# Optimization experiments

Hardware: AMD Instinct MI355X
Metric: run time of the kernel (lower is better)

Reference implementation:

```python
import jax, jax.numpy as jnp
import numpy as np


def setup_inputs() -> dict:
    key = jax.random.key(0)
    k1, k2, k3 = jax.random.split(key, 3)
    B, N, L, H, E = 4, 4, 1024, 8, 64
    queries = jax.random.normal(k1, (B, N, L, H, E), dtype=jnp.float32)
    keys = jax.random.normal(k2, (B, N, L, H, E), dtype=jnp.float32)
    values = jax.random.normal(k3, (B, N, L, H, E), dtype=jnp.float32)
    return {"queries": queries, "keys": keys, "values": values}


def reference(queries, keys, values):
    B, N, L, H, E = queries.shape
    S = values.shape[2]
    scale = 1.0 / jnp.sqrt(jnp.asarray(E, queries.dtype))
    # scores: [B, N, H, L, S]
    scores = jnp.einsum('bnlhe,bnshe->bnhls', queries, keys)
    # causal mask: True above the diagonal (future positions), broadcast over b,n,h
    causal = jnp.triu(jnp.ones((L, S), dtype=bool), k=1)
    scores = jnp.where(causal, -jnp.inf, scores)
    A = jax.nn.softmax(scale * scores, axis=-1)  # dropout p=0.0 -> identity
    V = jnp.einsum('bnhls,bnshd->bnlhd', A, values)
    return V
```

## Files before the change

### kernel.cpp

```cpp
#include <hip/hip_runtime.h>
#include <hip/hip_bf16.h>


typedef __bf16 bf16x8 __attribute__((ext_vector_type(8)));
typedef __bf16 bf16x4 __attribute__((ext_vector_type(4)));
typedef float  f32x4  __attribute__((ext_vector_type(4)));
typedef unsigned u32x2 __attribute__((ext_vector_type(2)));
typedef unsigned u32x4 __attribute__((ext_vector_type(4)));

#define SEQ 1024
#define ROWSTRIDE 512

__device__ inline bf16x8 pack8(float4 a, float4 b) {
    bf16x8 f;
    f[0]=(__bf16)a.x; f[1]=(__bf16)a.y; f[2]=(__bf16)a.z; f[3]=(__bf16)a.w;
    f[4]=(__bf16)b.x; f[5]=(__bf16)b.y; f[6]=(__bf16)b.z; f[7]=(__bf16)b.w;
    return f;
}

__device__ inline bf16x8 pack8s(float4 a, float4 b, float s) {
    bf16x8 f;
    f[0]=(__bf16)(a.x*s); f[1]=(__bf16)(a.y*s); f[2]=(__bf16)(a.z*s); f[3]=(__bf16)(a.w*s);
    f[4]=(__bf16)(b.x*s); f[5]=(__bf16)(b.y*s); f[6]=(__bf16)(b.z*s); f[7]=(__bf16)(b.w*s);
    return f;
}

__device__ inline void lds_barrier() {
    asm volatile("s_waitcnt lgkmcnt(0)\n\ts_barrier" ::: "memory");
}

__device__ inline void swap32(unsigned &a, unsigned &b) {
    asm("v_permlane32_swap_b32 %0, %1" : "+v"(a), "+v"(b));
}
__device__ inline void swap16(unsigned &a, unsigned &b) {
    asm("v_permlane16_swap_b32 %0, %1" : "+v"(a), "+v"(b));
}

__global__ __launch_bounds__(256) void attn_fwd(
    const float* __restrict__ Qg,
    const float* __restrict__ Kg,
    const float* __restrict__ Vg,
    float* __restrict__ Og)
{
    __shared__ __bf16 Kds[2][64][64];
    __shared__ __bf16 Vds[2][64][64];

    const int blk  = blockIdx.x;
    const int qt   = blk >> 7;
    const int head = blk & 127;
    const int h    = head & 7;
    const int bn   = head >> 3;

    const int tid  = threadIdx.x;
    const int wave = tid >> 6;
    const int lane = tid & 63;
    const int quad = lane >> 4;
    const int l15  = lane & 15;
    const int swz  = l15 & 7;

    const size_t base = (size_t)bn * SEQ * ROWSTRIDE + (size_t)h * 64;

    const float kscale = 0.125f * 1.44269504088896f;

    const int qrow = qt * 128 + wave * 32;
    bf16x8 qa[2][2];
    #pragma unroll
    for (int qh = 0; qh < 2; ++qh) {
        const float* qp = Qg + base + (size_t)(qrow + qh * 16 + l15) * ROWSTRIDE + quad * 8;
        #pragma unroll
        for (int t = 0; t < 2; ++t)
            qa[qh][t] = pack8s(*(const float4*)(qp + t * 32),
                               *(const float4*)(qp + t * 32 + 4), kscale);
    }

    f32x4 o[2][4];
    float lsum[2] = {0.f, 0.f};
    #pragma unroll
    for (int qh = 0; qh < 2; ++qh)
        #pragma unroll
        for (int e = 0; e < 4; ++e) o[qh][e] = (f32x4){0.f, 0.f, 0.f, 0.f};

    const int sr = tid >> 2, cbk = (tid & 3) << 1;
    const int ve = tid & 63, cbv = (tid >> 6) << 1;

    const int ntiles = 2 * qt + 2;

    const float* kp = Kg + base + (size_t)sr * ROWSTRIDE + (cbk << 3);
    const float* vp = Vg + base + (size_t)(cbv << 3) * ROWSTRIDE + ve;

    float4 kpre[4];
    float  vpre[16];
    #pragma unroll
    for (int i = 0; i < 4; ++i) kpre[i] = *(const float4*)(kp + i * 4);
    #pragma unroll
    for (int j = 0; j < 16; ++j) vpre[j] = vp[(size_t)j * ROWSTRIDE];
    kp += (size_t)64 * ROWSTRIDE;
    vp += (size_t)64 * ROWSTRIDE;

    for (int tile = 0; tile < ntiles; ++tile) {
        const int bb = tile & 1;

        {
            const int rk = sr & 7;
            *(bf16x8*)&Kds[bb][sr][(cbk ^ rk) << 3]       = pack8(kpre[0], kpre[1]);
            *(bf16x8*)&Kds[bb][sr][((cbk + 1) ^ rk) << 3] = pack8(kpre[2], kpre[3]);
            bf16x8 f0, f1;
            #pragma unroll
            for (int jj = 0; jj < 8; ++jj) { f0[jj] = (__bf16)vpre[jj]; f1[jj] = (__bf16)vpre[8 + jj]; }
            const int rv = ve & 7;
            *(bf16x8*)&Vds[bb][ve][(cbv ^ rv) << 3]       = f0;
            *(bf16x8*)&Vds[bb][ve][((cbv + 1) ^ rv) << 3] = f1;
        }

        if (tile + 1 < ntiles) {
            #pragma unroll
            for (int i = 0; i < 4; ++i) kpre[i] = *(const float4*)(kp + i * 4);
            #pragma unroll
            for (int j = 0; j < 16; ++j) vpre[j] = vp[(size_t)j * ROWSTRIDE];
            kp += (size_t)64 * ROWSTRIDE;
            vp += (size_t)64 * ROWSTRIDE;
        }

        lds_barrier();

        const int relq = tile * 64 - qrow;
        const bool active   = relq < 32;
        const bool hiActive = relq < 0;

        bf16x8 pf[2][2];

        auto phase = [&](int ph) {
            f32x4 sacc[2][2];
            #pragma unroll
            for (int qh = 0; qh < 2; ++qh)
                #pragma unroll
                for (int cl = 0; cl < 2; ++cl) sacc[qh][cl] = (f32x4){0.f, 0.f, 0.f, 0.f};
            __builtin_amdgcn_s_setprio(1);
            #pragma unroll
            for (int cl = 0; cl < 2; ++cl) {
                #pragma unroll
                for (int t = 0; t < 2; ++t) {
                    bf16x8 kb = *(const bf16x8*)&Kds[bb][(ph * 2 + cl) * 16 + l15][((t * 4 + quad) ^ swz) << 3];
                    sacc[0][cl] = __builtin_amdgcn_mfma_f32_16x16x32_bf16(kb, qa[0][t], sacc[0][cl], 0, 0, 0);
                    sacc[1][cl] = __builtin_amdgcn_mfma_f32_16x16x32_bf16(kb, qa[1][t], sacc[1][cl], 0, 0, 0);
                }
            }
            __builtin_amdgcn_s_setprio(0);
            const int pm = relq + ph * 32;
            #pragma unroll
            for (int qh = 0; qh < 2; ++qh) {
                unsigned U[2][2];
                float ls = 0.f;
                if (pm == 0) {
                    #pragma unroll
                    for (int cl = 0; cl < 2; ++cl) {
                        bf16x4 pk;
                        #pragma unroll
                        for (int r = 0; r < 4; ++r) {
                            float p = __builtin_amdgcn_exp2f(sacc[qh][cl][r]);
                            if (cl * 16 + quad * 4 + r > qh * 16 + l15) p = 0.f;
                            ls += p; pk[r] = (__bf16)p;
                        }
                        u32x2 uu = __builtin_bit_cast(u32x2, pk);
                        U[cl][0] = uu[0]; U[cl][1] = uu[1];
                    }
                } else {
                    #pragma unroll
                    for (int cl = 0; cl < 2; ++cl) {
                        bf16x4 pk;
                        #pragma unroll
                        for (int r = 0; r < 4; ++r) {
                            float p = __builtin_amdgcn_exp2f(sacc[qh][cl][r]);
                            ls += p; pk[r] = (__bf16)p;
                        }
                        u32x2 uu = __builtin_bit_cast(u32x2, pk);
                        U[cl][0] = uu[0]; U[cl][1] = uu[1];
                    }
                }
                lsum[qh] += ls;
                unsigned a0 = U[0][0], a1 = U[0][1];
                unsigned b0 = U[1][0], b1 = U[1][1];
                swap32(a0, b0); swap32(a1, b1);
                swap16(a0, b0); swap16(a1, b1);
                u32x4 w; w[0] = a0; w[1] = a1; w[2] = b0; w[3] = b1;
                pf[qh][ph] = __builtin_bit_cast(bf16x8, w);
            }
        };

        if (active) {
            phase(0);
            if (hiActive) phase(1);

            __builtin_amdgcn_s_setprio(1);
            #pragma unroll
            for (int e = 0; e < 4; ++e) {
                bf16x8 vb0 = *(const bf16x8*)&Vds[bb][e * 16 + l15][(quad ^ swz) << 3];
                o[0][e] = __builtin_amdgcn_mfma_f32_16x16x32_bf16(vb0, pf[0][0], o[0][e], 0, 0, 0);
                o[1][e] = __builtin_amdgcn_mfma_f32_16x16x32_bf16(vb0, pf[1][0], o[1][e], 0, 0, 0);
                if (hiActive) {
                    bf16x8 vb1 = *(const bf16x8*)&Vds[bb][e * 16 + l15][((4 + quad) ^ swz) << 3];
                    o[0][e] = __builtin_amdgcn_mfma_f32_16x16x32_bf16(vb1, pf[0][1], o[0][e], 0, 0, 0);
                    o[1][e] = __builtin_amdgcn_mfma_f32_16x16x32_bf16(vb1, pf[1][1], o[1][e], 0, 0, 0);
                }
            }
            __builtin_amdgcn_s_setprio(0);
        }
    }

    #pragma unroll
    for (int qh = 0; qh < 2; ++qh) {
        float s = lsum[qh];
        s += __shfl_xor(s, 16);
        s += __shfl_xor(s, 32);
        const float inv_l = 1.f / s;
        float* op = Og + base + (size_t)(qrow + qh * 16 + l15) * ROWSTRIDE + quad * 4;
        #pragma unroll
        for (int e = 0; e < 4; ++e) {
            float4 v;
            v.x = o[qh][e][0] * inv_l;
            v.y = o[qh][e][1] * inv_l;
            v.z = o[qh][e][2] * inv_l;
            v.w = o[qh][e][3] * inv_l;
            *(float4*)(op + e * 16) = v;
        }
    }
}

extern "C" void kernel_launch(void* const* d_in, const int* in_sizes, int n_in,
                              void* d_out, int out_size, void* d_ws, size_t ws_size,
                              hipStream_t stream) {
    const float* Qg = (const float*)d_in[0];
    const float* Kg = (const float*)d_in[1];
    const float* Vg = (const float*)d_in[2];
    float* Og = (float*)d_out;
    attn_fwd<<<dim3(1024), dim3(256), 0, stream>>>(Qg, Kg, Vg, Og);
}
```

Before: 155.5 us.

## Double query tile per block to 256 rows with 8 waves and reversed tile order

Each block now covers 256 query rows with 512 threads (8 waves) instead of 128 rows with 256 threads, so every K/V tile staged in LDS is reused by twice as many waves and global K/V traffic per query drops. The grid shrinks to 512 blocks, and the second half of the grid takes the query tiles in reverse order to even out causal work across launch order. The per-thread K/V staging loads are halved and the softmax/pack code is moved into a helper. In exchange, fewer and larger blocks may lower occupancy and make load balance coarser, and the per-block causal imbalance between early and late waves grows.

```diff
diff --git a/kernel.cpp b/kernel.cpp
--- a/kernel.cpp
+++ b/kernel.cpp
@@ -36,7 +36,39 @@
     asm("v_permlane16_swap_b32 %0, %1" : "+v"(a), "+v"(b));
 }
 
-__global__ __launch_bounds__(256) void attn_fwd(
+__device__ inline bf16x8 softmax_pack(f32x4 sA, f32x4 sB, bool diag,
+                                      int qloc, int quad, float &ls)
+{
+    unsigned U0a, U0b, U1a, U1b;
+    {
+        bf16x4 pk;
+        #pragma unroll
+        for (int r = 0; r < 4; ++r) {
+            float p = __builtin_amdgcn_exp2f(sA[r]);
+            p = (diag && (quad * 4 + r > qloc)) ? 0.f : p;
+            ls += p; pk[r] = (__bf16)p;
+        }
+        u32x2 uu = __builtin_bit_cast(u32x2, pk);
+        U0a = uu[0]; U0b = uu[1];
+    }
+    {
+        bf16x4 pk;
+        #pragma unroll
+        for (int r = 0; r < 4; ++r) {
+            float p = __builtin_amdgcn_exp2f(sB[r]);
+            p = (diag && (16 + quad * 4 + r > qloc)) ? 0.f : p;
+            ls += p; pk[r] = (__bf16)p;
+        }
+        u32x2 uu = __builtin_bit_cast(u32x2, pk);
+        U1a = uu[0]; U1b = uu[1];
+    }
+    swap32(U0a, U1a); swap32(U0b, U1b);
+    swap16(U0a, U1a); swap16(U0b, U1b);
+    u32x4 w; w[0] = U0a; w[1] = U0b; w[2] = U1a; w[3] = U1b;
+    return __builtin_bit_cast(bf16x8, w);
+}
+
+__global__ __launch_bounds__(512) void attn_fwd(
     const float* __restrict__ Qg,
     const float* __restrict__ Kg,
     const float* __restrict__ Vg,
@@ -46,10 +78,10 @@
     __shared__ __bf16 Vds[2][64][64];
 
     const int blk  = blockIdx.x;
-    const int qt   = blk >> 7;
     const int head = blk & 127;
     const int h    = head & 7;
     const int bn   = head >> 3;
+    const int qt   = (blk < 256) ? (blk >> 7) : (3 - ((blk & 255) >> 7));
 
     const int tid  = threadIdx.x;
     const int wave = tid >> 6;
@@ -62,7 +94,7 @@
 
     const float kscale = 0.125f * 1.44269504088896f;
 
-    const int qrow = qt * 128 + wave * 32;
+    const int qrow = qt * 256 + wave * 32;
     bf16x8 qa[2][2];
     #pragma unroll
     for (int qh = 0; qh < 2; ++qh) {
@@ -74,49 +106,45 @@
     }
 
     f32x4 o[2][4];
-    float lsum[2] = {0.f, 0.f};
+    float lsum0 = 0.f, lsum1 = 0.f;
     #pragma unroll
     for (int qh = 0; qh < 2; ++qh)
         #pragma unroll
         for (int e = 0; e < 4; ++e) o[qh][e] = (f32x4){0.f, 0.f, 0.f, 0.f};
 
-    const int sr = tid >> 2, cbk = (tid & 3) << 1;
-    const int ve = tid & 63, cbv = (tid >> 6) << 1;
-
-    const int ntiles = 2 * qt + 2;
-
-    const float* kp = Kg + base + (size_t)sr * ROWSTRIDE + (cbk << 3);
-    const float* vp = Vg + base + (size_t)(cbv << 3) * ROWSTRIDE + ve;
-
-    float4 kpre[4];
-    float  vpre[16];
-    #pragma unroll
-    for (int i = 0; i < 4; ++i) kpre[i] = *(const float4*)(kp + i * 4);
-    #pragma unroll
-    for (int j = 0; j < 16; ++j) vpre[j] = vp[(size_t)j * ROWSTRIDE];
+    const int sr = tid >> 3, kc = tid & 7;
+    const int ve = tid & 63;
+
+    const int ntiles = 4 * qt + 4;
+
+    const float* kp = Kg + base + (size_t)sr * ROWSTRIDE + kc * 8;
+    const float* vp = Vg + base + (size_t)(wave * 8) * ROWSTRIDE + ve;
+
+    float4 kpre[2];
+    float  vpre[8];
+    kpre[0] = *(const float4*)kp;
+    kpre[1] = *(const float4*)(kp + 4);
+    #pragma unroll
+    for (int j = 0; j < 8; ++j) vpre[j] = vp[(size_t)j * ROWSTRIDE];
     kp += (size_t)64 * ROWSTRIDE;
     vp += (size_t)64 * ROWSTRIDE;
 
     for (int tile = 0; tile < ntiles; ++tile) {
         const int bb = tile & 1;
 
+        *(bf16x8*)&Kds[bb][sr][(kc ^ (sr & 7)) << 3] = pack8(kpre[0], kpre[1]);
         {
-            const int rk = sr & 7;
-            *(bf16x8*)&Kds[bb][sr][(cbk ^ rk) << 3]       = pack8(kpre[0], kpre[1]);
-            *(bf16x8*)&Kds[bb][sr][((cbk + 1) ^ rk) << 3] = pack8(kpre[2], kpre[3]);
-            bf16x8 f0, f1;
+            bf16x8 f0;
             #pragma unroll
-            for (int jj = 0; jj < 8; ++jj) { f0[jj] = (__bf16)vpre[jj]; f1[jj] = (__bf16)vpre[8 + jj]; }
-            const int rv = ve & 7;
-            *(bf16x8*)&Vds[bb][ve][(cbv ^ rv) << 3]       = f0;
-            *(bf16x8*)&Vds[bb][ve][((cbv + 1) ^ rv) << 3] = f1;
+            for (int jj = 0; jj < 8; ++jj) f0[jj] = (__bf16)vpre[jj];
+            *(bf16x8*)&Vds[bb][ve][(wave ^ (ve & 7)) << 3] = f0;
         }
 
         if (tile + 1 < ntiles) {
+            kpre[0] = *(const float4*)kp;
+            kpre[1] = *(const float4*)(kp + 4);
             #pragma unroll
-            for (int i = 0; i < 4; ++i) kpre[i] = *(const float4*)(kp + i * 4);
-            #pragma unroll
-            for (int j = 0; j < 16; ++j) vpre[j] = vp[(size_t)j * ROWSTRIDE];
+            for (int j = 0; j < 8; ++j) vpre[j] = vp[(size_t)j * ROWSTRIDE];
             kp += (size_t)64 * ROWSTRIDE;
             vp += (size_t)64 * ROWSTRIDE;
         }
@@ -127,80 +155,56 @@
         const bool active   = relq < 32;
         const bool hiActive = relq < 0;
 
-        bf16x8 pf[2][2];
-
-        auto phase = [&](int ph) {
-            f32x4 sacc[2][2];
-            #pragma unroll
-            for (int qh = 0; qh < 2; ++qh)
-                #pragma unroll
-                for (int cl = 0; cl < 2; ++cl) sacc[qh][cl] = (f32x4){0.f, 0.f, 0.f, 0.f};
-            __builtin_amdgcn_s_setprio(1);
-            #pragma unroll
-            for (int cl = 0; cl < 2; ++cl) {
+        bf16x8 pf00 = {}, pf01 = {}, pf10 = {}, pf11 = {};
+
+        if (active) {
+            {
+                f32x4 s00 = (f32x4){0.f,0.f,0.f,0.f}, s01 = (f32x4){0.f,0.f,0.f,0.f};
+                f32x4 s10 = (f32x4){0.f,0.f,0.f,0.f}, s11 = (f32x4){0.f,0.f,0.f,0.f};
+                __builtin_amdgcn_s_setprio(1);
                 #pragma unroll
                 for (int t = 0; t < 2; ++t) {
-                    bf16x8 kb = *(const bf16x8*)&Kds[bb][(ph * 2 + cl) * 16 + l15][((t * 4 + quad) ^ swz) << 3];
-                    sacc[0][cl] = __builtin_amdgcn_mfma_f32_16x16x32_bf16(kb, qa[0][t], sacc[0][cl], 0, 0, 0);
-                    sacc[1][cl] = __builtin_amdgcn_mfma_f32_16x16x32_bf16(kb, qa[1][t], sacc[1][cl], 0, 0, 0);
+                    bf16x8 kb0 = *(const bf16x8*)&Kds[bb][ 0 + l15][((t * 4 + quad) ^ swz) << 3];
+                    bf16x8 kb1 = *(const bf16x8*)&Kds[bb][16 + l15][((t * 4 + quad) ^ swz) << 3];
+                    s00 = __builtin_amdgcn_mfma_f32_16x16x32_bf16(kb0, qa[0][t], s00, 0, 0, 0);
+                    s10 = __builtin_amdgcn_mfma_f32_16x16x32_bf16(kb0, qa[1][t], s10, 0, 0, 0);
+                    s01 = __builtin_amdgcn_mfma_f32_16x16x32_bf16(kb1, qa[0][t], s01, 0, 0, 0);
+                    s11 = __builtin_amdgcn_mfma_f32_16x16x32_bf16(kb1, qa[1][t], s11, 0, 0, 0);
                 }
+                __builtin_amdgcn_s_setprio(0);
+                const bool diag0 = (relq == 0);
+                pf00 = softmax_pack(s00, s01, diag0, l15,      quad, lsum0);
+                pf10 = softmax_pack(s10, s11, diag0, 16 + l15, quad, lsum1);
             }
-            __builtin_amdgcn_s_setprio(0);
-            const int pm = relq + ph * 32;
-            #pragma unroll
-            for (int qh = 0; qh < 2; ++qh) {
-                unsigned U[2][2];
-                float ls = 0.f;
-                if (pm == 0) {
-                    #pragma unroll
-                    for (int cl = 0; cl < 2; ++cl) {
-                        bf16x4 pk;
-                        #pragma unroll
-                        for (int r = 0; r < 4; ++r) {
-                            float p = __builtin_amdgcn_exp2f(sacc[qh][cl][r]);
-                            if (cl * 16 + quad * 4 + r > qh * 16 + l15) p = 0.f;
-                            ls += p; pk[r] = (__bf16)p;
-                        }
-                        u32x2 uu = __builtin_bit_cast(u32x2, pk);
-                        U[cl][0] = uu[0]; U[cl][1] = uu[1];
-                    }
-                } else {
-                    #pragma unroll
-                    for (int cl = 0; cl < 2; ++cl) {
-                        bf16x4 pk;
-                        #pragma unroll
-                        for (int r = 0; r < 4; ++r) {
-                            float p = __builtin_amdgcn_exp2f(sacc[qh][cl][r]);
-                            ls += p; pk[r] = (__bf16)p;
-                        }
-                        u32x2 uu = __builtin_bit_cast(u32x2, pk);
-                        U[cl][0] = uu[0]; U[cl][1] = uu[1];
-                    }
+            if (hiActive) {
+                f32x4 s00 = (f32x4){0.f,0.f,0.f,0.f}, s01 = (f32x4){0.f,0.f,0.f,0.f};
+                f32x4 s10 = (f32x4){0.f,0.f,0.f,0.f}, s11 = (f32x4){0.f,0.f,0.f,0.f};
+                __builtin_amdgcn_s_setprio(1);
+                #pragma unroll
+                for (int t = 0; t < 2; ++t) {
+                    bf16x8 kb0 = *(const bf16x8*)&Kds[bb][32 + l15][((t * 4 + quad) ^ swz) << 3];
+                    bf16x8 kb1 = *(const bf16x8*)&Kds[bb][48 + l15][((t * 4 + quad) ^ swz) << 3];
+                    s00 = __builtin_amdgcn_mfma_f32_16x16x32_bf16(kb0, qa[0][t], s00, 0, 0, 0);
+                    s10 = __builtin_amdgcn_mfma_f32_16x16x32_bf16(kb0, qa[1][t], s10, 0, 0, 0);
+                    s01 = __builtin_amdgcn_mfma_f32_16x16x32_bf16(kb1, qa[0][t], s01, 0, 0, 0);
+                    s11 = __builtin_amdgcn_mfma_f32_16x16x32_bf16(kb1, qa[1][t], s11, 0, 0, 0);
                 }
-                lsum[qh] += ls;
-                unsigned a0 = U[0][0], a1 = U[0][1];
-                unsigned b0 = U[1][0], b1 = U[1][1];
-                swap32(a0, b0); swap32(a1, b1);
-                swap16(a0, b0); swap16(a1, b1);
-                u32x4 w; w[0] = a0; w[1] = a1; w[2] = b0; w[3] = b1;
-                pf[qh][ph] = __builtin_bit_cast(bf16x8, w);
+                __builtin_amdgcn_s_setprio(0);
+                const bool diag1 = (relq == -32);
+                pf01 = softmax_pack(s00, s01, diag1, l15,      quad, lsum0);
+                pf11 = softmax_pack(s10, s11, diag1, 16 + l15, quad, lsum1);
             }
-        };
-
-        if (active) {
-            phase(0);
-            if (hiActive) phase(1);
 
             __builtin_amdgcn_s_setprio(1);
             #pragma unroll
             for (int e = 0; e < 4; ++e) {
                 bf16x8 vb0 = *(const bf16x8*)&Vds[bb][e * 16 + l15][(quad ^ swz) << 3];
-                o[0][e] = __builtin_amdgcn_mfma_f32_16x16x32_bf16(vb0, pf[0][0], o[0][e], 0, 0, 0);
-                o[1][e] = __builtin_amdgcn_mfma_f32_16x16x32_bf16(vb0, pf[1][0], o[1][e], 0, 0, 0);
+                o[0][e] = __builtin_amdgcn_mfma_f32_16x16x32_bf16(vb0, pf00, o[0][e], 0, 0, 0);
+                o[1][e] = __builtin_amdgcn_mfma_f32_16x16x32_bf16(vb0, pf10, o[1][e], 0, 0, 0);
                 if (hiActive) {
                     bf16x8 vb1 = *(const bf16x8*)&Vds[bb][e * 16 + l15][((4 + quad) ^ swz) << 3];
-                    o[0][e] = __builtin_amdgcn_mfma_f32_16x16x32_bf16(vb1, pf[0][1], o[0][e], 0, 0, 0);
-                    o[1][e] = __builtin_amdgcn_mfma_f32_16x16x32_bf16(vb1, pf[1][1], o[1][e], 0, 0, 0);
+                    o[0][e] = __builtin_amdgcn_mfma_f32_16x16x32_bf16(vb1, pf01, o[0][e], 0, 0, 0);
+                    o[1][e] = __builtin_amdgcn_mfma_f32_16x16x32_bf16(vb1, pf11, o[1][e], 0, 0, 0);
                 }
             }
             __builtin_amdgcn_s_setprio(0);
@@ -209,7 +213,7 @@
 
     #pragma unroll
     for (int qh = 0; qh < 2; ++qh) {
-        float s = lsum[qh];
+        float s = qh ? lsum1 : lsum0;
         s += __shfl_xor(s, 16);
         s += __shfl_xor(s, 32);
         const float inv_l = 1.f / s;
@@ -233,5 +237,5 @@
     const float* Kg = (const float*)d_in[1];
     const float* Vg = (const float*)d_in[2];
     float* Og = (float*)d_out;
-    attn_fwd<<<dim3(1024), dim3(256), 0, stream>>>(Qg, Kg, Vg, Og);
-}
+    attn_fwd<<<dim3(512), dim3(512), 0, stream>>>(Qg, Kg, Vg, Og);
+}
```

Result: faster. 146.3 us (-5.9%).
